# Kernel tuning notes

Hardware: AMD Instinct MI355X
Metric: run time of the kernel (lower is better)

Reference implementation:

```python
import jax, jax.numpy as jnp
import numpy as np

B, S, F, H = 2, 1024, 1024, 16  # H = n_heads arg; effective chunks Hc = F // H = 64, head_dim = H = 16


def _lin(x, w, b):
    # torch nn.Linear: y = x @ W^T + b, W has shape (out, in)
    return jnp.einsum('bsf,of->bso', x, w) + b


def setup_inputs() -> dict:
    key = jax.random.key(0)
    ks = jax.random.split(key, 16)
    sc = 0.02
    d = {'x': jax.random.normal(ks[0], (B, S, F), jnp.float32)}
    names = ['wq', 'wk', 'wv', 'vq', 'vk', 'vv', 'wo']
    for i, n in enumerate(names):
        d[n + '_w'] = jax.random.normal(ks[1 + 2 * i], (F, F), jnp.float32) * sc
        d[n + '_b'] = jax.random.normal(ks[2 + 2 * i], (F,), jnp.float32) * sc
    return d


def reference(x, wq_w, wq_b, wk_w, wk_b, wv_w, wv_b,
              vq_w, vq_b, vk_w, vk_b, vv_w, vv_b, wo_w, wo_b):
    b, s, f = x.shape
    hc = f // H  # number of chunks produced by torch.split(., n_heads, dim=-1)
    q = _lin(_lin(x, wq_w, wq_b), vq_w, vq_b)
    k = _lin(_lin(x, wk_w, wk_b), vk_w, vk_b)
    v = _lin(_lin(x, wv_w, wv_b), vv_w, vv_b)
    # split into hc chunks of size H along feature dim, concat on batch dim -> (hc, b, s, H)
    q = q.reshape(b, s, hc, H).transpose(2, 0, 1, 3)
    k = k.reshape(b, s, hc, H).transpose(2, 0, 1, 3)
    v = v.reshape(b, s, hc, H).transpose(2, 0, 1, 3)
    scale = jnp.sqrt(jnp.asarray(H, q.dtype))
    scores = jnp.einsum('cbqh,cbkh->cbqk', q, k) / scale  # (hc, b, s, s)
    attn = jax.nn.softmax(scores, axis=-1)
    o = jnp.einsum('cbqk,cbkh->cbqh', attn, v)  # (hc, b, s, H)
    # torch: view(H, b, s, f//H) then unsqueeze(-2).swapaxes(0,-2).reshape(b,s,f)
    o = o.reshape(H, b, s, hc).transpose(1, 2, 0, 3).reshape(b, s, f)
    return _lin(o, wo_w, wo_b)
```

## Files before the change

### kernel.cpp

```cpp
#include <hip/hip_runtime.h>
#include <hip/hip_bf16.h>
#include <stdint.h>

typedef __bf16 bf16_t;
typedef __bf16 bf16x8 __attribute__((ext_vector_type(8)));
typedef __bf16 bf16x4 __attribute__((ext_vector_type(4)));
typedef float f32x4 __attribute__((ext_vector_type(4)));
typedef float f32x16 __attribute__((ext_vector_type(16)));
typedef uint32_t u32x4 __attribute__((ext_vector_type(4)));

#define XN 2097152
#define WN 1048576

static __device__ __forceinline__ uint16_t bfbits(float f) {
    bf16_t b = (bf16_t)f;
    return __builtin_bit_cast(uint16_t, b);
}

__global__ void cast_all_k(const float* __restrict__ x,
    const float* __restrict__ w0, const float* __restrict__ w1, const float* __restrict__ w2,
    const float* __restrict__ w3, const float* __restrict__ w4, const float* __restrict__ w5,
    const float* __restrict__ w6, bf16_t* __restrict__ dst)
{
    const int TOTC = (XN + 7 * WN) / 4;
    for (int c = blockIdx.x * blockDim.x + threadIdx.x; c < TOTC; c += gridDim.x * blockDim.x) {
        int el = c * 4;
        const float* s;
        if (el < XN) {
            s = x + el;
        } else {
            int r = el - XN;
            int wi = r >> 20;
            int off = r & (WN - 1);
            const float* wp = (wi == 0) ? w0 : (wi == 1) ? w1 : (wi == 2) ? w2
                             : (wi == 3) ? w3 : (wi == 4) ? w4 : (wi == 5) ? w5 : w6;
            s = wp + off;
        }
        float4 f = *(const float4*)s;
        bf16x4 o = { (bf16_t)f.x, (bf16_t)f.y, (bf16_t)f.z, (bf16_t)f.w };
        *(bf16x4*)(dst + el) = o;
    }
}

template<int EPI>
__global__ __launch_bounds__(256)
void gemm128(const bf16_t* __restrict__ A0, const bf16_t* __restrict__ A1, const bf16_t* __restrict__ A2,
             const bf16_t* __restrict__ W0, const bf16_t* __restrict__ W1, const bf16_t* __restrict__ W2,
             const float* __restrict__ bias0, const float* __restrict__ bias1, const float* __restrict__ bias2,
             void* O0, void* O1, void* O2)
{
    const int z = blockIdx.z;
    const bf16_t* A = (z == 0) ? A0 : (z == 1) ? A1 : A2;
    const bf16_t* W = (z == 0) ? W0 : (z == 1) ? W1 : W2;
    const float* bias = (z == 0) ? bias0 : (z == 1) ? bias1 : bias2;
    void* Ov = (z == 0) ? O0 : (z == 1) ? O1 : O2;

    __shared__ bf16_t As[128][72];
    __shared__ bf16_t Bs[128][72];

    const int tid = threadIdx.x;
    const int lane = tid & 63, wave = tid >> 6;
    const int lo = lane & 15, hi = lane >> 4;
    const int wr = wave >> 1, wc = wave & 1;
    const int m0 = blockIdx.y * 128, n0 = blockIdx.x * 128;

    f32x4 acc[4][4] = {};

    for (int kt = 0; kt < 16; ++kt) {
        const int K0 = kt * 64;
        bf16x8 ra[4], rb[4];
#pragma unroll
        for (int i = 0; i < 4; ++i) {
            int cid = tid + i * 256;
            int row = cid >> 3, ko = cid & 7;
            ra[i] = *(const bf16x8*)(A + (size_t)(m0 + row) * 1024 + K0 + ko * 8);
            rb[i] = *(const bf16x8*)(W + (size_t)(n0 + row) * 1024 + K0 + ko * 8);
        }
        __syncthreads();
#pragma unroll
        for (int i = 0; i < 4; ++i) {
            int cid = tid + i * 256;
            int row = cid >> 3, ko = cid & 7;
            *(bf16x8*)&As[row][ko * 8] = ra[i];
            *(bf16x8*)&Bs[row][ko * 8] = rb[i];
        }
        __syncthreads();
#pragma unroll
        for (int kk = 0; kk < 2; ++kk) {
            const int kb = kk * 32 + hi * 8;
            bf16x8 af[4], bfr[4];
#pragma unroll
            for (int m = 0; m < 4; ++m) af[m] = *(const bf16x8*)&As[wr * 64 + m * 16 + lo][kb];
#pragma unroll
            for (int n = 0; n < 4; ++n) bfr[n] = *(const bf16x8*)&Bs[wc * 64 + n * 16 + lo][kb];
#pragma unroll
            for (int m = 0; m < 4; ++m)
#pragma unroll
                for (int n = 0; n < 4; ++n)
                    acc[m][n] = __builtin_amdgcn_mfma_f32_16x16x32_bf16(af[m], bfr[n], acc[m][n], 0, 0, 0);
        }
    }

#pragma unroll
    for (int n = 0; n < 4; ++n) {
        const int col = n0 + wc * 64 + n * 16 + lo;
        const float bv = bias[col];
#pragma unroll
        for (int m = 0; m < 4; ++m) {
            const int r0 = m0 + wr * 64 + m * 16 + hi * 4;
            if (EPI == 2) {
                float* O = (float*)Ov;
#pragma unroll
                for (int r = 0; r < 4; ++r)
                    O[(size_t)(r0 + r) * 1024 + col] = acc[m][n][r] + bv;
            } else if (EPI == 0 || z < 2) {
                bf16_t* O = (bf16_t*)Ov;
#pragma unroll
                for (int r = 0; r < 4; ++r)
                    O[(size_t)(r0 + r) * 1024 + col] = (bf16_t)(acc[m][n][r] + bv);
            } else {
                bf16_t* O = (bf16_t*)Ov;
                int cch = col >> 4, h = col & 15;
                int bb = r0 >> 10, ss = r0 & 1023;
                bf16x4 pv = { (bf16_t)(acc[m][n][0] + bv), (bf16_t)(acc[m][n][1] + bv),
                              (bf16_t)(acc[m][n][2] + bv), (bf16_t)(acc[m][n][3] + bv) };
                *(bf16x4*)(O + ((size_t)((cch * 2 + bb) * 16 + h)) * 1024 + ss) = pv;
            }
        }
    }
}

__global__ __launch_bounds__(256)
void attn_k(const bf16_t* __restrict__ qg, const bf16_t* __restrict__ kg,
            const bf16_t* __restrict__ vtg, bf16_t* __restrict__ y)
{
    const int c = blockIdx.y, b = blockIdx.z;
    const int lane = threadIdx.x & 63, wave = threadIdx.x >> 6;
    const int l31 = lane & 31, hi = lane >> 5;
    const int s = blockIdx.x * 128 + wave * 32 + l31;

    bf16x8 qf = *(const bf16x8*)(qg + ((size_t)(b * 1024 + s)) * 1024 + c * 16 + hi * 8);
    const bf16_t* kbase = kg + ((size_t)b * 1024) * 1024 + c * 16 + hi * 8;
    const bf16_t* vbase = vtg + ((size_t)((c * 2 + b) * 16 + (lane & 15))) * 1024 + hi * 8;

    f32x16 oacc = {};
    const f32x16 zero16 = {};
    float den = 0.f;

    for (int jt = 0; jt < 32; ++jt) {
        bf16x8 kf = *(const bf16x8*)(kbase + (size_t)(jt * 32 + l31) * 1024);
        f32x16 st = __builtin_amdgcn_mfma_f32_32x32x16_bf16(kf, qf, zero16, 0, 0, 0);

        float p[16];
#pragma unroll
        for (int r = 0; r < 16; ++r) { p[r] = __expf(st[r] * 0.25f); den += p[r]; }

        uint32_t pk[8];
#pragma unroll
        for (int w = 0; w < 8; ++w)
            pk[w] = (uint32_t)bfbits(p[2 * w]) | ((uint32_t)bfbits(p[2 * w + 1]) << 16);
        uint32_t sp[8];
#pragma unroll
        for (int w = 0; w < 8; ++w) sp[w] = (uint32_t)__shfl_xor((int)pk[w], 32, 64);

        uint32_t a0, a1, a2, a3, b0, b1, b2, b3;
        if (hi) {
            a0 = sp[2]; a1 = sp[3]; a2 = pk[2]; a3 = pk[3];
            b0 = sp[6]; b1 = sp[7]; b2 = pk[6]; b3 = pk[7];
        } else {
            a0 = pk[0]; a1 = pk[1]; a2 = sp[0]; a3 = sp[1];
            b0 = pk[4]; b1 = pk[5]; b2 = sp[4]; b3 = sp[5];
        }
        u32x4 f0v = { a0, a1, a2, a3 };
        u32x4 f1v = { b0, b1, b2, b3 };
        bf16x8 pf0 = __builtin_bit_cast(bf16x8, f0v);
        bf16x8 pf1 = __builtin_bit_cast(bf16x8, f1v);

        bf16x8 vf0 = *(const bf16x8*)(vbase + jt * 32);
        bf16x8 vf1 = *(const bf16x8*)(vbase + jt * 32 + 16);
        oacc = __builtin_amdgcn_mfma_f32_32x32x16_bf16(vf0, pf0, oacc, 0, 0, 0);
        oacc = __builtin_amdgcn_mfma_f32_32x32x16_bf16(vf1, pf1, oacc, 0, 0, 0);
    }

    float dtot = den + __shfl_xor(den, 32, 64);
    float rinv = 1.0f / dtot;

    const int bo = (c >> 1) & 1;
    const int so = (c & 1) * 512 + b * 256 + (s >> 2);
    const int f0i = (c >> 2) * 64 + (s & 3) * 16;
    bf16_t* yb = y + ((size_t)bo * 1024 + so) * 1024 + f0i + 4 * hi;
    bf16x4 o1 = { (bf16_t)(oacc[0] * rinv), (bf16_t)(oacc[1] * rinv),
                  (bf16_t)(oacc[2] * rinv), (bf16_t)(oacc[3] * rinv) };
    *(bf16x4*)(yb) = o1;
    bf16x4 o2 = { (bf16_t)(oacc[4] * rinv), (bf16_t)(oacc[5] * rinv),
                  (bf16_t)(oacc[6] * rinv), (bf16_t)(oacc[7] * rinv) };
    *(bf16x4*)(yb + 8) = o2;
}

extern "C" void kernel_launch(void* const* d_in, const int* in_sizes, int n_in,
                              void* d_out, int out_size, void* d_ws, size_t ws_size,
                              hipStream_t stream)
{
    (void)in_sizes; (void)n_in; (void)out_size; (void)ws_size;
    const float* x    = (const float*)d_in[0];
    const float* wq_b = (const float*)d_in[2];
    const float* wk_b = (const float*)d_in[4];
    const float* wv_b = (const float*)d_in[6];
    const float* vq_b = (const float*)d_in[8];
    const float* vk_b = (const float*)d_in[10];
    const float* vv_b = (const float*)d_in[12];
    const float* wo_b = (const float*)d_in[14];

    bf16_t* base = (bf16_t*)d_ws;
    bf16_t* xbf = base;
    bf16_t* wbf = base + XN;
    bf16_t* q1  = base + XN + 7 * WN;
    bf16_t* k1  = q1 + XN;
    bf16_t* v1  = k1 + XN;
    bf16_t* q   = v1 + XN;
    bf16_t* k   = q + XN;
    bf16_t* vT  = k + XN;
    bf16_t* y   = q1;

    cast_all_k<<<dim3(2048), dim3(256), 0, stream>>>(
        x, (const float*)d_in[1], (const float*)d_in[3], (const float*)d_in[5],
        (const float*)d_in[7], (const float*)d_in[9], (const float*)d_in[11],
        (const float*)d_in[13], base);

    gemm128<0><<<dim3(8, 16, 3), dim3(256), 0, stream>>>(
        xbf, xbf, xbf, wbf, wbf + WN, wbf + 2 * WN,
        wq_b, wk_b, wv_b, q1, k1, v1);

    gemm128<1><<<dim3(8, 16, 3), dim3(256), 0, stream>>>(
        q1, k1, v1, wbf + 3 * WN, wbf + 4 * WN, wbf + 5 * WN,
        vq_b, vk_b, vv_b, q, k, vT);

    attn_k<<<dim3(8, 64, 2), dim3(256), 0, stream>>>(q, k, vT, y);

    gemm128<2><<<dim3(8, 16, 1), dim3(256), 0, stream>>>(
        y, y, y, wbf + 6 * WN, wbf + 6 * WN, wbf + 6 * WN,
        wo_b, wo_b, wo_b, d_out, d_out, d_out);
}
```

Measured before the change: 218.9 us.

## Use direct global-to-LDS loads in GEMM and prefetch K/V in attention

The GEMM tile staging now uses global_load_lds so data goes straight to shared memory instead of through registers. The padded LDS layout is dropped, which may bring back bank conflicts on the fragment reads. The attention kernel prefetches the next K/V fragments one iteration ahead and folds the softmax scale and log2(e) into the Q projection epilogue, so it can call exp2f. It also halves the number of cross-lane shuffles by exchanging only the needed halves.

```diff
diff --git a/kernel.cpp b/kernel.cpp
--- a/kernel.cpp
+++ b/kernel.cpp
@@ -11,6 +11,9 @@
 
 #define XN 2097152
 #define WN 1048576
+
+typedef __attribute__((address_space(1))) const uint8_t* gas_ptr;
+typedef __attribute__((address_space(3))) uint8_t* las_ptr;
 
 static __device__ __forceinline__ uint16_t bfbits(float f) {
     bf16_t b = (bf16_t)f;
@@ -42,6 +45,8 @@
     }
 }
 
+#define QSCALE 0.36067376022224085f
+
 template<int EPI>
 __global__ __launch_bounds__(256)
 void gemm128(const bf16_t* __restrict__ A0, const bf16_t* __restrict__ A1, const bf16_t* __restrict__ A2,
@@ -55,8 +60,8 @@
     const float* bias = (z == 0) ? bias0 : (z == 1) ? bias1 : bias2;
     void* Ov = (z == 0) ? O0 : (z == 1) ? O1 : O2;
 
-    __shared__ bf16_t As[128][72];
-    __shared__ bf16_t Bs[128][72];
+    __shared__ bf16_t As[128 * 64];
+    __shared__ bf16_t Bs[128 * 64];
 
     const int tid = threadIdx.x;
     const int lane = tid & 63, wave = tid >> 6;
@@ -68,21 +73,16 @@
 
     for (int kt = 0; kt < 16; ++kt) {
         const int K0 = kt * 64;
-        bf16x8 ra[4], rb[4];
+        __syncthreads();
 #pragma unroll
         for (int i = 0; i < 4; ++i) {
-            int cid = tid + i * 256;
-            int row = cid >> 3, ko = cid & 7;
-            ra[i] = *(const bf16x8*)(A + (size_t)(m0 + row) * 1024 + K0 + ko * 8);
-            rb[i] = *(const bf16x8*)(W + (size_t)(n0 + row) * 1024 + K0 + ko * 8);
-        }
-        __syncthreads();
-#pragma unroll
-        for (int i = 0; i < 4; ++i) {
-            int cid = tid + i * 256;
-            int row = cid >> 3, ko = cid & 7;
-            *(bf16x8*)&As[row][ko * 8] = ra[i];
-            *(bf16x8*)&Bs[row][ko * 8] = rb[i];
+            const int cbase = i * 256 + wave * 64;
+            const int c = cbase + lane;
+            const int row = c >> 3, ko = c & 7;
+            const bf16_t* ga = A + (size_t)(m0 + row) * 1024 + K0 + ko * 8;
+            const bf16_t* gb = W + (size_t)(n0 + row) * 1024 + K0 + ko * 8;
+            __builtin_amdgcn_global_load_lds((gas_ptr)ga, (las_ptr)(As + cbase * 8), 16, 0, 0);
+            __builtin_amdgcn_global_load_lds((gas_ptr)gb, (las_ptr)(Bs + cbase * 8), 16, 0, 0);
         }
         __syncthreads();
 #pragma unroll
@@ -90,9 +90,9 @@
             const int kb = kk * 32 + hi * 8;
             bf16x8 af[4], bfr[4];
 #pragma unroll
-            for (int m = 0; m < 4; ++m) af[m] = *(const bf16x8*)&As[wr * 64 + m * 16 + lo][kb];
-#pragma unroll
-            for (int n = 0; n < 4; ++n) bfr[n] = *(const bf16x8*)&Bs[wc * 64 + n * 16 + lo][kb];
+            for (int m = 0; m < 4; ++m) af[m] = *(const bf16x8*)&As[(wr * 64 + m * 16 + lo) * 64 + kb];
+#pragma unroll
+            for (int n = 0; n < 4; ++n) bfr[n] = *(const bf16x8*)&Bs[(wc * 64 + n * 16 + lo) * 64 + kb];
 #pragma unroll
             for (int m = 0; m < 4; ++m)
 #pragma unroll
@@ -115,9 +115,10 @@
                     O[(size_t)(r0 + r) * 1024 + col] = acc[m][n][r] + bv;
             } else if (EPI == 0 || z < 2) {
                 bf16_t* O = (bf16_t*)Ov;
+                const float sc = (EPI == 1 && z == 0) ? QSCALE : 1.0f;
 #pragma unroll
                 for (int r = 0; r < 4; ++r)
-                    O[(size_t)(r0 + r) * 1024 + col] = (bf16_t)(acc[m][n][r] + bv);
+                    O[(size_t)(r0 + r) * 1024 + col] = (bf16_t)((acc[m][n][r] + bv) * sc);
             } else {
                 bf16_t* O = (bf16_t*)Ov;
                 int cch = col >> 4, h = col & 15;
@@ -140,46 +141,56 @@
     const int s = blockIdx.x * 128 + wave * 32 + l31;
 
     bf16x8 qf = *(const bf16x8*)(qg + ((size_t)(b * 1024 + s)) * 1024 + c * 16 + hi * 8);
-    const bf16_t* kbase = kg + ((size_t)b * 1024) * 1024 + c * 16 + hi * 8;
-    const bf16_t* vbase = vtg + ((size_t)((c * 2 + b) * 16 + (lane & 15))) * 1024 + hi * 8;
+    const bf16_t* kptr = kg + ((size_t)(b * 1024 + l31)) * 1024 + c * 16 + hi * 8;
+    const bf16_t* vptr = vtg + ((size_t)((c * 2 + b) * 16 + (lane & 15))) * 1024 + hi * 8;
 
     f32x16 oacc = {};
-    const f32x16 zero16 = {};
+    const f32x16 z16 = {};
     float den = 0.f;
 
+    bf16x8 kf = *(const bf16x8*)(kptr);
+    bf16x8 vf0 = *(const bf16x8*)(vptr);
+    bf16x8 vf1 = *(const bf16x8*)(vptr + 16);
+
+#pragma unroll 2
     for (int jt = 0; jt < 32; ++jt) {
-        bf16x8 kf = *(const bf16x8*)(kbase + (size_t)(jt * 32 + l31) * 1024);
-        f32x16 st = __builtin_amdgcn_mfma_f32_32x32x16_bf16(kf, qf, zero16, 0, 0, 0);
+        const int jn = (jt + 1) & 31;
+        bf16x8 kn  = *(const bf16x8*)(kptr + (size_t)jn * 32768);
+        bf16x8 vn0 = *(const bf16x8*)(vptr + jn * 32);
+        bf16x8 vn1 = *(const bf16x8*)(vptr + jn * 32 + 16);
+
+        f32x16 st = __builtin_amdgcn_mfma_f32_32x32x16_bf16(kf, qf, z16, 0, 0, 0);
 
         float p[16];
 #pragma unroll
-        for (int r = 0; r < 16; ++r) { p[r] = __expf(st[r] * 0.25f); den += p[r]; }
+        for (int r = 0; r < 16; ++r) { p[r] = exp2f(st[r]); den += p[r]; }
 
         uint32_t pk[8];
 #pragma unroll
         for (int w = 0; w < 8; ++w)
             pk[w] = (uint32_t)bfbits(p[2 * w]) | ((uint32_t)bfbits(p[2 * w + 1]) << 16);
-        uint32_t sp[8];
-#pragma unroll
-        for (int w = 0; w < 8; ++w) sp[w] = (uint32_t)__shfl_xor((int)pk[w], 32, 64);
-
-        uint32_t a0, a1, a2, a3, b0, b1, b2, b3;
-        if (hi) {
-            a0 = sp[2]; a1 = sp[3]; a2 = pk[2]; a3 = pk[3];
-            b0 = sp[6]; b1 = sp[7]; b2 = pk[6]; b3 = pk[7];
-        } else {
-            a0 = pk[0]; a1 = pk[1]; a2 = sp[0]; a3 = sp[1];
-            b0 = pk[4]; b1 = pk[5]; b2 = sp[4]; b3 = sp[5];
-        }
-        u32x4 f0v = { a0, a1, a2, a3 };
-        u32x4 f1v = { b0, b1, b2, b3 };
+
+        uint32_t t0 = hi ? pk[0] : pk[2];
+        uint32_t t1 = hi ? pk[1] : pk[3];
+        uint32_t t2 = hi ? pk[4] : pk[6];
+        uint32_t t3 = hi ? pk[5] : pk[7];
+        t0 = (uint32_t)__shfl_xor((int)t0, 32, 64);
+        t1 = (uint32_t)__shfl_xor((int)t1, 32, 64);
+        t2 = (uint32_t)__shfl_xor((int)t2, 32, 64);
+        t3 = (uint32_t)__shfl_xor((int)t3, 32, 64);
+
+        u32x4 f0v, f1v;
+        f0v[0] = hi ? t0 : pk[0];  f0v[1] = hi ? t1 : pk[1];
+        f0v[2] = hi ? pk[2] : t0;  f0v[3] = hi ? pk[3] : t1;
+        f1v[0] = hi ? t2 : pk[4];  f1v[1] = hi ? t3 : pk[5];
+        f1v[2] = hi ? pk[6] : t2;  f1v[3] = hi ? pk[7] : t3;
         bf16x8 pf0 = __builtin_bit_cast(bf16x8, f0v);
         bf16x8 pf1 = __builtin_bit_cast(bf16x8, f1v);
 
-        bf16x8 vf0 = *(const bf16x8*)(vbase + jt * 32);
-        bf16x8 vf1 = *(const bf16x8*)(vbase + jt * 32 + 16);
         oacc = __builtin_amdgcn_mfma_f32_32x32x16_bf16(vf0, pf0, oacc, 0, 0, 0);
         oacc = __builtin_amdgcn_mfma_f32_32x32x16_bf16(vf1, pf1, oacc, 0, 0, 0);
+
+        kf = kn; vf0 = vn0; vf1 = vn1;
     }
 
     float dtot = den + __shfl_xor(den, 32, 64);
```

Result: slower. 229.8 us (+5.0%).
